# Kernel optimization log

Measured on AMD Instinct MI355X. Metric: run time of the kernel, lower is better.

## Reference

```python
import jax, jax.numpy as jnp
import numpy as np

N_NODES = 100000


def gcn_conv(x, W, b, src, dst, n):
    # PyG GCNConv: linear transform, add self-loops, symmetric deg^-1/2 norm,
    # scatter-sum messages from src -> dst, add bias.
    x = x @ W  # [N, out]
    loop = jnp.arange(n, dtype=src.dtype)
    src_sl = jnp.concatenate([src, loop])
    dst_sl = jnp.concatenate([dst, loop])
    deg = jax.ops.segment_sum(jnp.ones_like(dst_sl, dtype=x.dtype), dst_sl, num_segments=n)
    dinv = jax.lax.rsqrt(deg)
    norm = dinv[src_sl] * dinv[dst_sl]  # [E+N]
    msg = x[src_sl] * norm[:, None]
    out = jax.ops.segment_sum(msg, dst_sl, num_segments=n)
    return out + b


def base_gnn(x, edge_index, W1, b1, W2, b2):
    src, dst = edge_index[0], edge_index[1]
    n = x.shape[0]
    h = gcn_conv(x, W1, b1, src, dst, n)
    h = jax.nn.relu(h)
    return gcn_conv(h, W2, b2, src, dst, n)


def setup_inputs() -> dict:
    key = jax.random.key(0)
    ks = jax.random.split(key, 12)
    n, e, ep, en = N_NODES, 1600000, 200000, 200000
    in_ch, hid, out_ch, n_classes = 256, 128, 128, 10
    x = jax.random.normal(ks[0], (n, in_ch), dtype=jnp.float32)
    edge_index = jax.random.randint(ks[1], (2, e), 0, n, dtype=jnp.int64)
    edge_index_pos = jax.random.randint(ks[2], (2, ep), 0, n, dtype=jnp.int64)
    edge_index_neg = jax.random.randint(ks[3], (2, en), 0, n, dtype=jnp.int64)
    s1 = 1.0 / np.sqrt(in_ch)
    s2 = 1.0 / np.sqrt(hid)
    so = 1.0 / np.sqrt(out_ch)
    sl = 1.0 / np.sqrt(2 * out_ch)
    return {
        "x": x,
        "edge_index": edge_index,
        "edge_index_pos": edge_index_pos,
        "edge_index_neg": edge_index_neg,
        "W1": jax.random.uniform(ks[4], (in_ch, hid), jnp.float32, -s1, s1),
        "b1": jnp.zeros((hid,), jnp.float32),
        "W2": jax.random.uniform(ks[5], (hid, out_ch), jnp.float32, -s2, s2),
        "b2": jnp.zeros((out_ch,), jnp.float32),
        "Wcls": jax.random.uniform(ks[6], (out_ch, n_classes), jnp.float32, -so, so),
        "bcls": jax.random.uniform(ks[7], (n_classes,), jnp.float32, -so, so),
        "Wlink": jax.random.uniform(ks[8], (2 * out_ch, 1), jnp.float32, -sl, sl),
        "blink": jax.random.uniform(ks[9], (1,), jnp.float32, -sl, sl),
    }


def reference(x, edge_index, edge_index_pos, edge_index_neg,
              W1, b1, W2, b2, Wcls, bcls, Wlink, blink):
    # Shared base embedding (math identical to torch's redundant recompute)
    h = base_gnn(x, edge_index, W1, b1, W2, b2)  # [N, 128]
    # Node head
    node_logits = jax.nn.relu(h) @ Wcls + bcls
    node_pred = jax.nn.log_softmax(node_logits, axis=1)
    # Link head: gather endpoint embeddings, concat, linear
    xp = jnp.concatenate([h[edge_index_pos[0]], h[edge_index_pos[1]]], axis=1)
    xn = jnp.concatenate([h[edge_index_neg[0]], h[edge_index_neg[1]]], axis=1)
    link_pos = (xp @ Wlink + blink)[:, 0]
    link_neg = (xn @ Wlink + blink)[:, 0]
    return (node_pred, link_pos, link_neg)
```

## Files before the change

kernel.cpp:

```cpp
#include <hip/hip_runtime.h>
#include <stdint.h>

typedef __attribute__((ext_vector_type(8))) short bf16x8;
typedef __attribute__((ext_vector_type(4))) float f32x4;

__device__ __forceinline__ float b2f(uint32_t h) {
    union { uint32_t u; float f; } v; v.u = h << 16; return v.f;
}
__device__ __forceinline__ ushort f2b(float f) {
    union { float f; uint32_t u; } v; v.f = f;
    uint32_t u = v.u;
    return (ushort)((u + 0x7fffu + ((u >> 16) & 1u)) >> 16);
}
__device__ __forceinline__ float ldin(const void* p, int i, int fp32) {
    return fp32 ? ((const float*)p)[i] : b2f(((const ushort*)p)[i]);
}

__device__ __forceinline__ void sniff(const void* W1, const void* ei, int* sf) {
    if (threadIdx.x < 64) {
        int l = threadIdx.x;
        const ushort* w = (const ushort*)W1;
        bool bad = !(fabsf(b2f(w[l])) <= 0.25f) || !(fabsf(b2f(w[64 + l])) <= 0.25f);
        unsigned long long mb = __ballot(bad);
        const int* e = (const int*)ei;
        bool z = (l < 16) ? (e[2 * l + 1] == 0) : false;
        unsigned long long mz = __ballot(z);
        if (l == 0) {
            sf[0] = mb ? 1 : 0;
            sf[1] = (__popcll(mz & 0xffffull) >= 15) ? 1 : 0;
        }
    }
    __syncthreads();
}


__global__ __launch_bounds__(256) void k_prep(const void* ei, const void* ep, const void* en,
                                              const void* W1, const void* b1, const void* W2,
                                              const void* b2, const void* Wc, const void* bc,
                                              const void* Wl, const void* bl,
                                              int* cEi, int* cEp, int* cEn,
                                              ushort* Wt1, ushort* Wt2, ushort* WtC,
                                              ushort* b1c, ushort* b2c, ushort* bcc,
                                              ushort* Wlc, ushort* blc,
                                              int* __restrict__ histM,
                                              int twoEp, int twoEn, int N,
                                              int E, int NB1,
                                              int Bidx, int Bw) {
    __shared__ int sf[2];
    __shared__ int h[512];
    sniff(W1, ei, sf);
    int f = sf[0], i64 = sf[1];
    int b = blockIdx.x;

    if (b < Bidx) {
        int i = (b * 256 + threadIdx.x) * 2;
        const void* srcp; int* dstp; int j = i;
        if (i < E) { srcp = ei; dstp = cEi; }
        else if (i < E + twoEp) { srcp = ep; dstp = cEp; j = i - E; }
        else if (i < E + twoEp + twoEn) { srcp = en; dstp = cEn; j = i - E - twoEp; }
        else return;
        int v0, v1;
        if (i64) {
            longlong2 t = *(const longlong2*)((const long long*)srcp + j);
            v0 = (int)t.x; v1 = (int)t.y;
        } else {
            int2 t = *(const int2*)((const int*)srcp + j);
            v0 = t.x; v1 = t.y;
        }
        v0 = v0 < 0 ? 0 : (v0 >= N ? N - 1 : v0);
        v1 = v1 < 0 ? 0 : (v1 >= N ? N - 1 : v1);
        *(int2*)(dstp + j) = make_int2(v0, v1);
    } else if (b < Bidx + Bw) {
        int i = (b - Bidx) * 256 + threadIdx.x;
        if (i < 32768) {
            int c = i >> 8, kpos = i & 255;
            int s = kpos >> 5, t = kpos & 31, q = t >> 3, jj = t & 7;
            int k = s * 32 + (jj < 4 ? q * 4 + jj : 16 + q * 4 + (jj - 4));
            Wt1[i] = f2b(ldin(W1, k * 128 + c, f));
        } else if (i < 49152) {
            int j = i - 32768, c = j >> 7, k = j & 127;
            Wt2[j] = f2b(ldin(W2, k * 128 + c, f));
        } else if (i < 51200) {
            int j = i - 49152, c = j >> 7, k = j & 127;
            ushort v = 0;
            if (c < 10) v = f2b(ldin(Wc, k * 10 + c, f));
            WtC[j] = v;
        } else if (i < 51328) {
            int j = i - 51200; b1c[j] = f2b(ldin(b1, j, f));
        } else if (i < 51456) {
            int j = i - 51328; b2c[j] = f2b(ldin(b2, j, f));
        } else if (i < 51472) {
            int j = i - 51456;
            ushort v = 0;
            if (j < 10) v = f2b(ldin(bc, j, f));
            bcc[j] = v;
        } else if (i < 51728) {
            int j = i - 51472; Wlc[j] = f2b(ldin(Wl, j, f));
        } else if (i < 51736) {
            int j = i - 51728;
            ushort v = 0;
            if (j < 1) v = f2b(ldin(bl, 0, f));
            blc[j] = v;
        }
    } else {
        int b2 = b - Bidx - Bw;
        for (int j = threadIdx.x; j < 512; j += 256) h[j] = 0;
        __syncthreads();
        int base = b2 * 4096;
        for (int j = threadIdx.x; j < 4096; j += 256) {
            int i = base + j;
            if (i < E) {
                int d = i64 ? (int)((const long long*)ei)[E + i] : ((const int*)ei)[E + i];
                d = d < 0 ? 0 : (d >= N ? N - 1 : d);
                cEi[E + i] = d;
                atomicAdd(&h[d >> 8], 1);
            }
        }
        __syncthreads();
        for (int j = threadIdx.x; j < 512; j += 256)
            histM[j * NB1 + b2] = h[j];
    }
}

__global__ __launch_bounds__(1024) void k_mscan_block(const int* __restrict__ in, int* __restrict__ out,
                                                      int* __restrict__ bsum, int len) {
    __shared__ int sh[1024];
    int t = threadIdx.x;
    int i = blockIdx.x * 1024 + t;
    int val = (i < len) ? in[i] : 0;
    sh[t] = val; __syncthreads();
    for (int off = 1; off < 1024; off <<= 1) {
        int v = (t >= off) ? sh[t - off] : 0;
        __syncthreads();
        sh[t] += v;
        __syncthreads();
    }
    if (i < len) out[i] = sh[t] - val;
    if (t == 1023) bsum[blockIdx.x] = sh[1023];
}

__global__ __launch_bounds__(1024) void k_mscan_topadd(int* __restrict__ out, const int* __restrict__ bsum,
                                                       int* __restrict__ cbs, int len, int mb,
                                                       int NB1, int E) {
    __shared__ int sh[1024];
    int t = threadIdx.x;
    sh[t] = (t < mb) ? bsum[t] : 0; __syncthreads();
    for (int off = 1; off < 1024; off <<= 1) {
        int v = (t >= off) ? sh[t - off] : 0;
        __syncthreads();
        sh[t] += v;
        __syncthreads();
    }
    int pref = (blockIdx.x > 0) ? sh[blockIdx.x - 1] : 0;
    int i = blockIdx.x * 1024 + t;
    if (i < len) {
        int v = out[i] + pref;
        out[i] = v;
        if (i % NB1 == 0) cbs[i / NB1] = v;
    }
    if (i == 0) cbs[512] = E;
}

__global__ __launch_bounds__(256) void k_scatter1(const int* __restrict__ src, const int* __restrict__ dst,
                                                  const int* __restrict__ off, int2* __restrict__ grouped,
                                                  int E, int NB1) {
    __shared__ int o[512];
    for (int j = threadIdx.x; j < 512; j += 256) o[j] = off[j * NB1 + blockIdx.x];
    __syncthreads();
    int base = blockIdx.x * 4096;
    for (int j = threadIdx.x; j < 4096; j += 256) {
        int i = base + j;
        if (i < E) {
            int d = dst[i];
            int p = atomicAdd(&o[d >> 8], 1);
            grouped[p] = make_int2(src[i], d);
        }
    }
}

__global__ __launch_bounds__(256) void k_degfill(const int2* __restrict__ grouped, const int* __restrict__ cbs,
                                                 int* __restrict__ rowptr, float* __restrict__ dinv,
                                                 int* __restrict__ edgeS, int N, int E) {
    __shared__ int cnt[256];
    __shared__ int obase[256];
    int t = threadIdx.x, b = blockIdx.x;
    cnt[t] = 0;
    __syncthreads();
    int s0 = cbs[b], s1 = cbs[b + 1];
    for (int i = s0 + t; i < s1; i += 256)
        atomicAdd(&cnt[grouped[i].y & 255], 1);
    __syncthreads();
    int deg = cnt[t];
    __syncthreads();
    for (int off = 1; off < 256; off <<= 1) {
        int vv = (t >= off) ? cnt[t - off] : 0;
        __syncthreads();
        cnt[t] += vv;
        __syncthreads();
    }
    int excl = cnt[t] - deg;
    int v = b * 256 + t;
    if (v < N) {
        rowptr[v] = s0 + excl;
        dinv[v] = rsqrtf((float)(deg + 1));
    }
    if (b == 0 && t == 0) rowptr[N] = E;
    obase[t] = s0 + excl;
    __syncthreads();
    for (int i = s0 + t; i < s1; i += 256) {
        int2 e = grouped[i];
        int p = atomicAdd(&obase[e.y & 255], 1);
        edgeS[p] = e.x;
    }
}

template <int NS, bool FUSE>
__global__ __launch_bounds__(256) void k_gemm(const void* __restrict__ Xraw,
                                              const ushort* __restrict__ Wt,
                                              ushort* __restrict__ Out, int nrows,
                                              const void* W1s, const void* eis) {
    __shared__ int sf[2];
    sniff(W1s, eis, sf);
    const bool f32in = FUSE && sf[0];

    __shared__ uint4 sB[NS * 8 * 64];
    const int tid = threadIdx.x;
    for (int it = tid; it < NS * 8 * 64; it += 256) {
        int l = it & 63, fn = it >> 6;
        int s = fn >> 3, n = fn & 7;
        int mr = l & 15, q = l >> 4;
        sB[it] = *(const uint4*)(Wt + (size_t)(n * 16 + mr) * (NS * 32) + s * 32 + q * 8);
    }
    __syncthreads();

    const int wave = tid >> 6;
    const int l = tid & 63;
    const int q = l >> 4, mr = l & 15;
    const int gw = blockIdx.x * 4 + wave;
    const int nw = gridDim.x * 4;
    const int ntile = (nrows + 15) >> 4;
    const int K = NS * 32;

    for (int tp = gw; tp * 4 < ntile; tp += nw) {
        const int t0 = tp * 4;
        const bool h1 = (t0 + 1 < ntile), h2 = (t0 + 2 < ntile), h3 = (t0 + 3 < ntile);
        const int tb1 = h1 ? t0 + 1 : t0, tb2 = h2 ? t0 + 2 : t0, tb3 = h3 ? t0 + 3 : t0;

        int r0 = t0 * 16 + mr;  if (r0 > nrows - 1) r0 = nrows - 1;
        int r1 = tb1 * 16 + mr; if (r1 > nrows - 1) r1 = nrows - 1;
        int r2 = tb2 * 16 + mr; if (r2 > nrows - 1) r2 = nrows - 1;
        int r3 = tb3 * 16 + mr; if (r3 > nrows - 1) r3 = nrows - 1;

        f32x4 accA[8], accB[8], accC[8], accD[8];
#pragma unroll
        for (int n = 0; n < 8; ++n) {
            accA[n] = (f32x4){0.f, 0.f, 0.f, 0.f};
            accB[n] = (f32x4){0.f, 0.f, 0.f, 0.f};
            accC[n] = (f32x4){0.f, 0.f, 0.f, 0.f};
            accD[n] = (f32x4){0.f, 0.f, 0.f, 0.f};
        }
#pragma unroll
        for (int s = 0; s < NS; ++s) {
            bf16x8 a0, a1, a2, a3;
            if (FUSE) {
                if (f32in) {
                    const float* x0 = (const float*)Xraw + (size_t)r0 * K + s * 32;
                    const float* x1 = (const float*)Xraw + (size_t)r1 * K + s * 32;
                    const float* x2 = (const float*)Xraw + (size_t)r2 * K + s * 32;
                    const float* x3 = (const float*)Xraw + (size_t)r3 * K + s * 32;
                    float4 lo, hi;
#define LOADCVT(dst, xp)                                                        \
                    lo = *(const float4*)((xp) + q * 4);                        \
                    hi = *(const float4*)((xp) + 16 + q * 4);                   \
                    dst[0] = (short)f2b(lo.x); dst[1] = (short)f2b(lo.y);       \
                    dst[2] = (short)f2b(lo.z); dst[3] = (short)f2b(lo.w);       \
                    dst[4] = (short)f2b(hi.x); dst[5] = (short)f2b(hi.y);       \
                    dst[6] = (short)f2b(hi.z); dst[7] = (short)f2b(hi.w);
                    LOADCVT(a0, x0) LOADCVT(a1, x1) LOADCVT(a2, x2) LOADCVT(a3, x3)
#undef LOADCVT
                } else {
                    const ushort* x0 = (const ushort*)Xraw + (size_t)r0 * K + s * 32;
                    const ushort* x1 = (const ushort*)Xraw + (size_t)r1 * K + s * 32;
                    const ushort* x2 = (const ushort*)Xraw + (size_t)r2 * K + s * 32;
                    const ushort* x3 = (const ushort*)Xraw + (size_t)r3 * K + s * 32;
                    uint2 lo, hi; uint4 m;
#define LOADB(dst, xp)                                                          \
                    lo = *(const uint2*)((xp) + q * 4);                         \
                    hi = *(const uint2*)((xp) + 16 + q * 4);                    \
                    m = (uint4){lo.x, lo.y, hi.x, hi.y};                        \
                    dst = __builtin_bit_cast(bf16x8, m);
                    LOADB(a0, x0) LOADB(a1, x1) LOADB(a2, x2) LOADB(a3, x3)
#undef LOADB
                }
            } else {
                const ushort* Xf = (const ushort*)Xraw;
                a0 = *(const bf16x8*)(Xf + ((size_t)t0 * NS * 64 + l) * 8 + s * 512);
                a1 = *(const bf16x8*)(Xf + ((size_t)tb1 * NS * 64 + l) * 8 + s * 512);
                a2 = *(const bf16x8*)(Xf + ((size_t)tb2 * NS * 64 + l) * 8 + s * 512);
                a3 = *(const bf16x8*)(Xf + ((size_t)tb3 * NS * 64 + l) * 8 + s * 512);
            }
#pragma unroll
            for (int n = 0; n < 8; ++n) {
                bf16x8 bfr = __builtin_bit_cast(bf16x8, sB[(s * 8 + n) * 64 + l]);
                accA[n] = __builtin_amdgcn_mfma_f32_16x16x32_bf16(bfr, a0, accA[n], 0, 0, 0);
                accB[n] = __builtin_amdgcn_mfma_f32_16x16x32_bf16(bfr, a1, accB[n], 0, 0, 0);
                accC[n] = __builtin_amdgcn_mfma_f32_16x16x32_bf16(bfr, a2, accC[n], 0, 0, 0);
                accD[n] = __builtin_amdgcn_mfma_f32_16x16x32_bf16(bfr, a3, accD[n], 0, 0, 0);
            }
        }
        {
            int row = t0 * 16 + mr;
            if (row < nrows) {
                ushort* orow = Out + (size_t)row * 128 + q * 4;
#pragma unroll
                for (int n = 0; n < 8; ++n) {
                    uint2 o;
                    o.x = (uint32_t)f2b(accA[n][0]) | ((uint32_t)f2b(accA[n][1]) << 16);
                    o.y = (uint32_t)f2b(accA[n][2]) | ((uint32_t)f2b(accA[n][3]) << 16);
                    *(uint2*)(orow + n * 16) = o;
                }
            }
        }
        if (h1) {
            int row = tb1 * 16 + mr;
            if (row < nrows) {
                ushort* orow = Out + (size_t)row * 128 + q * 4;
#pragma unroll
                for (int n = 0; n < 8; ++n) {
                    uint2 o;
                    o.x = (uint32_t)f2b(accB[n][0]) | ((uint32_t)f2b(accB[n][1]) << 16);
                    o.y = (uint32_t)f2b(accB[n][2]) | ((uint32_t)f2b(accB[n][3]) << 16);
                    *(uint2*)(orow + n * 16) = o;
                }
            }
        }
        if (h2) {
            int row = tb2 * 16 + mr;
            if (row < nrows) {
                ushort* orow = Out + (size_t)row * 128 + q * 4;
#pragma unroll
                for (int n = 0; n < 8; ++n) {
                    uint2 o;
                    o.x = (uint32_t)f2b(accC[n][0]) | ((uint32_t)f2b(accC[n][1]) << 16);
                    o.y = (uint32_t)f2b(accC[n][2]) | ((uint32_t)f2b(accC[n][3]) << 16);
                    *(uint2*)(orow + n * 16) = o;
                }
            }
        }
        if (h3) {
            int row = tb3 * 16 + mr;
            if (row < nrows) {
                ushort* orow = Out + (size_t)row * 128 + q * 4;
#pragma unroll
                for (int n = 0; n < 8; ++n) {
                    uint2 o;
                    o.x = (uint32_t)f2b(accD[n][0]) | ((uint32_t)f2b(accD[n][1]) << 16);
                    o.y = (uint32_t)f2b(accD[n][2]) | ((uint32_t)f2b(accD[n][3]) << 16);
                    *(uint2*)(orow + n * 16) = o;
                }
            }
        }
    }
}

__device__ __forceinline__ void fma8(float* acc, uint4 p, float w) {
    uint32_t pu[4] = {p.x, p.y, p.z, p.w};
#pragma unroll
    for (int k = 0; k < 4; ++k) {
        float lo = __uint_as_float(pu[k] << 16);
        float hi = __uint_as_float(pu[k] & 0xffff0000u);
        acc[2 * k]     += lo * w;
        acc[2 * k + 1] += hi * w;
    }
}

__global__ __launch_bounds__(256) void k_conv(const ushort* __restrict__ XW, const int* __restrict__ rowptr,
                                              const int* __restrict__ edgeS, const float* __restrict__ dinv,
                                              const ushort* __restrict__ bias, ushort* __restrict__ Hout,
                                              int n, int relu, int frag) {
    int wave = threadIdx.x >> 6;
    int v = blockIdx.x * 4 + wave;
    if (v >= n) return;
    int l = threadIdx.x & 63;
    int g = l >> 4;
    int c = l & 15;

    int s0 = rowptr[v], s1 = rowptr[v + 1];
    float dv = dinv[v];
    float wself = (g == 0) ? dv * dv : 0.f;

    uint4 pv = *(const uint4*)(XW + (size_t)v * 128 + c * 8);
    float acc[8];
    {
        uint32_t pu[4] = {pv.x, pv.y, pv.z, pv.w};
#pragma unroll
        for (int k = 0; k < 4; ++k) {
            acc[2 * k]     = __uint_as_float(pu[k] << 16) * wself;
            acc[2 * k + 1] = __uint_as_float(pu[k] & 0xffff0000u) * wself;
        }
    }

    int i = s0;
    while (i + 16 <= s1) {
        int sA = edgeS[i + g];
        int sB = edgeS[i + 4 + g];
        int sC = edgeS[i + 8 + g];
        int sD = edgeS[i + 12 + g];
        uint4 pA = *(const uint4*)(XW + (size_t)sA * 128 + c * 8);
        uint4 pB = *(const uint4*)(XW + (size_t)sB * 128 + c * 8);
        uint4 pC = *(const uint4*)(XW + (size_t)sC * 128 + c * 8);
        uint4 pD = *(const uint4*)(XW + (size_t)sD * 128 + c * 8);
        float wA = dinv[sA] * dv, wB = dinv[sB] * dv;
        float wC = dinv[sC] * dv, wD = dinv[sD] * dv;
        fma8(acc, pA, wA);
        fma8(acc, pB, wB);
        fma8(acc, pC, wC);
        fma8(acc, pD, wD);
        i += 16;
    }
    if (i + 8 <= s1) {
        int sA = edgeS[i + g];
        int sB = edgeS[i + 4 + g];
        uint4 pA = *(const uint4*)(XW + (size_t)sA * 128 + c * 8);
        uint4 pB = *(const uint4*)(XW + (size_t)sB * 128 + c * 8);
        float wA = dinv[sA] * dv, wB = dinv[sB] * dv;
        fma8(acc, pA, wA);
        fma8(acc, pB, wB);
        i += 8;
    }
    if (i + 4 <= s1) {
        int sA = edgeS[i + g];
        uint4 pA = *(const uint4*)(XW + (size_t)sA * 128 + c * 8);
        fma8(acc, pA, dinv[sA] * dv);
        i += 4;
    }
    if (i < s1) {
        int ei_ = i + g;
        bool val = ei_ < s1;
        int sA = edgeS[val ? ei_ : s0];
        uint4 pA = *(const uint4*)(XW + (size_t)sA * 128 + c * 8);
        fma8(acc, pA, val ? dinv[sA] * dv : 0.f);
    }

#pragma unroll
    for (int k = 0; k < 8; ++k) {
        acc[k] += __shfl_xor(acc[k], 16);
        acc[k] += __shfl_xor(acc[k], 32);
    }

    if (g == 0) {
        uint4 bb = *(const uint4*)(bias + c * 8);
        uint32_t bu[4] = {bb.x, bb.y, bb.z, bb.w};
        uint4 o;
        uint32_t* op = (uint32_t*)&o;
#pragma unroll
        for (int k = 0; k < 4; ++k) {
            float lo = acc[2 * k]     + __uint_as_float(bu[k] << 16);
            float hi = acc[2 * k + 1] + __uint_as_float(bu[k] & 0xffff0000u);
            if (relu) { lo = fmaxf(lo, 0.f); hi = fmaxf(hi, 0.f); }
            op[k] = (uint32_t)f2b(lo) | ((uint32_t)f2b(hi) << 16);
        }
        if (frag) {
            int tile = v >> 4, mr = v & 15;
            size_t chunk = ((size_t)(tile * 4 + (c >> 2)) * 64 + (c & 3) * 16 + mr);
            *(uint4*)(Hout + chunk * 8) = o;
        } else {
            *(uint4*)(Hout + (size_t)v * 128 + c * 8) = o;
        }
    }
}

__global__ __launch_bounds__(256) void k_nodehead(const ushort* __restrict__ H, const ushort* __restrict__ WtC,
                                                  const ushort* __restrict__ bcc, const ushort* __restrict__ Wlc,
                                                  float2* __restrict__ ab, void* __restrict__ out,
                                                  int n, const void* W1s, const void* eis) {
    __shared__ int sf[2];
    sniff(W1s, eis, sf);
    int fp32o = sf[0];
    int wave = threadIdx.x >> 6;
    int gw = blockIdx.x * 4 + wave;
    if (gw * 16 >= n) return;
    int l = threadIdx.x & 63;
    int q = l >> 4, mr = l & 15;
    int m0 = gw * 16;

    const ushort* hrow = H + (size_t)(m0 + mr) * 128 + q * 8;
    bf16x8 araw[4];
#pragma unroll
    for (int s = 0; s < 4; ++s) araw[s] = *(const bf16x8*)(hrow + s * 32);

    float pa = 0.f, pb = 0.f;
#pragma unroll
    for (int s = 0; s < 4; ++s) {
        bf16x8 w0 = *(const bf16x8*)(Wlc + s * 32 + q * 8);
        bf16x8 w1 = *(const bf16x8*)(Wlc + 128 + s * 32 + q * 8);
#pragma unroll
        for (int j = 0; j < 8; ++j) {
            float hv = b2f((ushort)araw[s][j]);
            pa += hv * b2f((ushort)w0[j]);
            pb += hv * b2f((ushort)w1[j]);
        }
    }
    pa += __shfl_xor(pa, 16); pa += __shfl_xor(pa, 32);
    pb += __shfl_xor(pb, 16); pb += __shfl_xor(pb, 32);
    if (q == 0 && (m0 + mr) < n) ab[m0 + mr] = make_float2(pa, pb);

    f32x4 acc = (f32x4){0.f, 0.f, 0.f, 0.f};
#pragma unroll
    for (int s = 0; s < 4; ++s) {
        bf16x8 a = araw[s];
#pragma unroll
        for (int j = 0; j < 8; ++j) {
            ushort t = (ushort)a[j];
            if (t & 0x8000u) a[j] = 0;
        }
        bf16x8 b = *(const bf16x8*)(WtC + (size_t)mr * 128 + s * 32 + q * 8);
        acc = __builtin_amdgcn_mfma_f32_16x16x32_bf16(a, b, acc, 0, 0, 0);
    }

    float bc = b2f(bcc[mr]);
#pragma unroll
    for (int r = 0; r < 4; ++r) {
        float logit = acc[r] + bc;
        float m = (mr < 10) ? logit : -1e30f;
#pragma unroll
        for (int off = 1; off < 16; off <<= 1) m = fmaxf(m, __shfl_xor(m, off, 16));
        float ex = (mr < 10) ? expf(logit - m) : 0.f;
        float ssum = ex;
#pragma unroll
        for (int off = 1; off < 16; off <<= 1) ssum += __shfl_xor(ssum, off, 16);
        int row = m0 + q * 4 + r;
        if (mr < 10 && row < n) {
            float lsm = logit - m - logf(ssum);
            size_t idx = (size_t)row * 10 + mr;
            if (fp32o) ((float*)out)[idx] = lsm;
            else ((ushort*)out)[idx] = f2b(lsm);
        }
    }
}

__global__ __launch_bounds__(256) void k_linkfast(const float2* __restrict__ ab, const int* __restrict__ pos,
                                                  const int* __restrict__ neg, const ushort* __restrict__ blc,
                                                  void* __restrict__ out, size_t obase, int Ep, int En,
                                                  const void* W1s, const void* eis) {
    __shared__ int sf[2];
    sniff(W1s, eis, sf);
    int i = blockIdx.x * 256 + threadIdx.x;
    if (i >= Ep + En) return;
    int s, d;
    if (i < Ep) { s = pos[i]; d = pos[Ep + i]; }
    else { int j = i - Ep; s = neg[j]; d = neg[En + j]; }
    float vf = ab[s].x + ab[d].y + b2f(blc[0]);
    size_t idx = obase + (size_t)i;
    if (sf[0]) ((float*)out)[idx] = vf;
    else ((ushort*)out)[idx] = f2b(vf);
}

extern "C" void kernel_launch(void* const* d_in, const int* in_sizes, int n_in,
                              void* d_out, int out_size, void* d_ws, size_t ws_size,
                              hipStream_t stream) {
    const void* x    = d_in[0];
    const void* ei   = d_in[1];
    const void* eip  = d_in[2];
    const void* ein  = d_in[3];
    const void* W1   = d_in[4];
    const void* b1   = d_in[5];
    const void* W2   = d_in[6];
    const void* b2   = d_in[7];
    const void* Wcls = d_in[8];
    const void* bcls = d_in[9];
    const void* Wl   = d_in[10];
    const void* bl   = d_in[11];

    const int N  = in_sizes[0] / 256;
    const int E  = in_sizes[1] / 2;
    const int Ep = in_sizes[2] / 2;
    const int En = in_sizes[3] / 2;

    const int NB1  = (E + 4095) / 4096;
    const int mlen = 512 * NB1;
    const int mb   = (mlen + 1023) / 1024;
    const int ntile = (N + 15) / 16;

    char* ws = (char*)d_ws;
    size_t off = 0;
    auto alloc = [&](size_t bytes) -> void* {
        void* p = ws + off;
        off = (off + bytes + 255) & ~(size_t)255;
        return p;
    };
    ushort* bufXW  = (ushort*)alloc((size_t)N * 128 * 2);
    ushort* bufH   = (ushort*)alloc((size_t)ntile * 4 * 64 * 16);
    float2* ab     = (float2*)alloc((size_t)N * 8);
    int*    cEi    = (int*)alloc((size_t)2 * E * 4);
    int*    cEp    = (int*)alloc((size_t)2 * Ep * 4);
    int*    cEn    = (int*)alloc((size_t)2 * En * 4);
    int2*   grouped= (int2*)alloc((size_t)E * 8);
    int*    histM  = (int*)alloc((size_t)mlen * 4);
    int*    offM   = (int*)alloc((size_t)mlen * 4);
    int*    msum   = (int*)alloc(4096);
    int*    cbs    = (int*)alloc(513 * 4);
    float*  dinv   = (float*)alloc((size_t)N * 4);
    int*    rowp   = (int*)alloc((size_t)(N + 1) * 4);
    int*    edgeS  = (int*)alloc((size_t)E * 4);
    ushort* Wt1    = (ushort*)alloc(65536);
    ushort* Wt2    = (ushort*)alloc(32768);
    ushort* WtC    = (ushort*)alloc(4096);
    ushort* b1c    = (ushort*)alloc(256);
    ushort* b2c    = (ushort*)alloc(256);
    ushort* bcc    = (ushort*)alloc(64);
    ushort* Wlc    = (ushort*)alloc(512);
    ushort* blc    = (ushort*)alloc(64);

    int twoEp = 2 * Ep, twoEn = 2 * En;
    int idx_total = E + twoEp + twoEn;
    int Bidx = (idx_total + 511) / 512;
    int Bw   = 203;

    k_prep<<<Bidx + Bw + NB1, 256, 0, stream>>>(ei, eip, ein, W1, b1, W2, b2, Wcls, bcls, Wl, bl,
                                                cEi, cEp, cEn, Wt1, Wt2, WtC,
                                                b1c, b2c, bcc, Wlc, blc, histM,
                                                twoEp, twoEn, N, E, NB1,
                                                Bidx, Bw);

    const int* srcp = cEi;
    const int* dstp = cEi + E;

    k_mscan_block<<<mb, 1024, 0, stream>>>(histM, offM, msum, mlen);
    k_mscan_topadd<<<mb, 1024, 0, stream>>>(offM, msum, cbs, mlen, mb, NB1, E);
    k_scatter1<<<NB1, 256, 0, stream>>>(srcp, dstp, offM, grouped, E, NB1);
    k_degfill<<<512, 256, 0, stream>>>(grouped, cbs, rowp, dinv, edgeS, N, E);

    int quads = (ntile + 3) / 4;
    int g1 = (quads + 3) / 4; if (g1 > 768) g1 = 768;
    k_gemm<8, true><<<g1, 256, 0, stream>>>(x, Wt1, bufXW, N, W1, ei);
    k_conv<<<(N + 3) / 4, 256, 0, stream>>>(bufXW, rowp, edgeS, dinv, b1c, bufH, N, 1, 1);
    k_gemm<4, false><<<g1, 256, 0, stream>>>(bufH, Wt2, bufXW, N, W1, ei);
    k_conv<<<(N + 3) / 4, 256, 0, stream>>>(bufXW, rowp, edgeS, dinv, b2c, bufH, N, 0, 0);

    int head_blocks = ((N + 15) / 16 + 3) / 4;
    k_nodehead<<<head_blocks, 256, 0, stream>>>(bufH, WtC, bcc, Wlc, ab, d_out, N, W1, ei);
    k_linkfast<<<(Ep + En + 255) / 256, 256, 0, stream>>>(ab, cEp, cEn, blc, d_out,
                                                          (size_t)N * 10, Ep, En, W1, ei);
}
```

Baseline: 447.4 us.

## Drop shared-memory weight staging and shrink GEMM tile to two row-tiles per wave

The GEMM kernel no longer copies the weight matrix into LDS at block start. Weight fragments are now read straight from global memory (expected to hit in L1/L2) inside the MFMA loop. Each wave now handles 2 row tiles instead of 4, which halves accumulator registers and may raise occupancy. The grid is no longer capped at 768 blocks, so it grows to cover all tile pairs. The trade-off is less reuse of each weight load and more global and cache traffic for the weights, in exchange for removing the LDS prologue and barrier and lowering register pressure.

```diff
diff --git a/kernel.cpp b/kernel.cpp
--- a/kernel.cpp
+++ b/kernel.cpp
@@ -223,16 +223,7 @@
     sniff(W1s, eis, sf);
     const bool f32in = FUSE && sf[0];
 
-    __shared__ uint4 sB[NS * 8 * 64];
     const int tid = threadIdx.x;
-    for (int it = tid; it < NS * 8 * 64; it += 256) {
-        int l = it & 63, fn = it >> 6;
-        int s = fn >> 3, n = fn & 7;
-        int mr = l & 15, q = l >> 4;
-        sB[it] = *(const uint4*)(Wt + (size_t)(n * 16 + mr) * (NS * 32) + s * 32 + q * 8);
-    }
-    __syncthreads();
-
     const int wave = tid >> 6;
     const int l = tid & 63;
     const int q = l >> 4, mr = l & 15;
@@ -241,33 +232,27 @@
     const int ntile = (nrows + 15) >> 4;
     const int K = NS * 32;
 
-    for (int tp = gw; tp * 4 < ntile; tp += nw) {
-        const int t0 = tp * 4;
-        const bool h1 = (t0 + 1 < ntile), h2 = (t0 + 2 < ntile), h3 = (t0 + 3 < ntile);
-        const int tb1 = h1 ? t0 + 1 : t0, tb2 = h2 ? t0 + 2 : t0, tb3 = h3 ? t0 + 3 : t0;
+    for (int tp = gw; tp * 2 < ntile; tp += nw) {
+        const int t0 = tp * 2;
+        const bool h1 = (t0 + 1 < ntile);
+        const int tb1 = h1 ? t0 + 1 : t0;
 
         int r0 = t0 * 16 + mr;  if (r0 > nrows - 1) r0 = nrows - 1;
         int r1 = tb1 * 16 + mr; if (r1 > nrows - 1) r1 = nrows - 1;
-        int r2 = tb2 * 16 + mr; if (r2 > nrows - 1) r2 = nrows - 1;
-        int r3 = tb3 * 16 + mr; if (r3 > nrows - 1) r3 = nrows - 1;
-
-        f32x4 accA[8], accB[8], accC[8], accD[8];
+
+        f32x4 accA[8], accB[8];
 #pragma unroll
         for (int n = 0; n < 8; ++n) {
             accA[n] = (f32x4){0.f, 0.f, 0.f, 0.f};
             accB[n] = (f32x4){0.f, 0.f, 0.f, 0.f};
-            accC[n] = (f32x4){0.f, 0.f, 0.f, 0.f};
-            accD[n] = (f32x4){0.f, 0.f, 0.f, 0.f};
         }
 #pragma unroll
         for (int s = 0; s < NS; ++s) {
-            bf16x8 a0, a1, a2, a3;
+            bf16x8 a0, a1;
             if (FUSE) {
                 if (f32in) {
                     const float* x0 = (const float*)Xraw + (size_t)r0 * K + s * 32;
                     const float* x1 = (const float*)Xraw + (size_t)r1 * K + s * 32;
-                    const float* x2 = (const float*)Xraw + (size_t)r2 * K + s * 32;
-                    const float* x3 = (const float*)Xraw + (size_t)r3 * K + s * 32;
                     float4 lo, hi;
 #define LOADCVT(dst, xp)                                                        \
                     lo = *(const float4*)((xp) + q * 4);                        \
@@ -276,36 +261,30 @@
                     dst[2] = (short)f2b(lo.z); dst[3] = (short)f2b(lo.w);       \
                     dst[4] = (short)f2b(hi.x); dst[5] = (short)f2b(hi.y);       \
                     dst[6] = (short)f2b(hi.z); dst[7] = (short)f2b(hi.w);
-                    LOADCVT(a0, x0) LOADCVT(a1, x1) LOADCVT(a2, x2) LOADCVT(a3, x3)
+                    LOADCVT(a0, x0) LOADCVT(a1, x1)
 #undef LOADCVT
                 } else {
                     const ushort* x0 = (const ushort*)Xraw + (size_t)r0 * K + s * 32;
                     const ushort* x1 = (const ushort*)Xraw + (size_t)r1 * K + s * 32;
-                    const ushort* x2 = (const ushort*)Xraw + (size_t)r2 * K + s * 32;
-                    const ushort* x3 = (const ushort*)Xraw + (size_t)r3 * K + s * 32;
                     uint2 lo, hi; uint4 m;
 #define LOADB(dst, xp)                                                          \
                     lo = *(const uint2*)((xp) + q * 4);                         \
                     hi = *(const uint2*)((xp) + 16 + q * 4);                    \
                     m = (uint4){lo.x, lo.y, hi.x, hi.y};                        \
                     dst = __builtin_bit_cast(bf16x8, m);
-                    LOADB(a0, x0) LOADB(a1, x1) LOADB(a2, x2) LOADB(a3, x3)
+                    LOADB(a0, x0) LOADB(a1, x1)
 #undef LOADB
                 }
             } else {
                 const ushort* Xf = (const ushort*)Xraw;
                 a0 = *(const bf16x8*)(Xf + ((size_t)t0 * NS * 64 + l) * 8 + s * 512);
                 a1 = *(const bf16x8*)(Xf + ((size_t)tb1 * NS * 64 + l) * 8 + s * 512);
-                a2 = *(const bf16x8*)(Xf + ((size_t)tb2 * NS * 64 + l) * 8 + s * 512);
-                a3 = *(const bf16x8*)(Xf + ((size_t)tb3 * NS * 64 + l) * 8 + s * 512);
             }
 #pragma unroll
             for (int n = 0; n < 8; ++n) {
-                bf16x8 bfr = __builtin_bit_cast(bf16x8, sB[(s * 8 + n) * 64 + l]);
+                bf16x8 bfr = *(const bf16x8*)(Wt + (size_t)(n * 16 + mr) * K + s * 32 + q * 8);
                 accA[n] = __builtin_amdgcn_mfma_f32_16x16x32_bf16(bfr, a0, accA[n], 0, 0, 0);
                 accB[n] = __builtin_amdgcn_mfma_f32_16x16x32_bf16(bfr, a1, accB[n], 0, 0, 0);
-                accC[n] = __builtin_amdgcn_mfma_f32_16x16x32_bf16(bfr, a2, accC[n], 0, 0, 0);
-                accD[n] = __builtin_amdgcn_mfma_f32_16x16x32_bf16(bfr, a3, accD[n], 0, 0, 0);
             }
         }
         {
@@ -330,32 +309,6 @@
                     uint2 o;
                     o.x = (uint32_t)f2b(accB[n][0]) | ((uint32_t)f2b(accB[n][1]) << 16);
                     o.y = (uint32_t)f2b(accB[n][2]) | ((uint32_t)f2b(accB[n][3]) << 16);
-                    *(uint2*)(orow + n * 16) = o;
-                }
-            }
-        }
-        if (h2) {
-            int row = tb2 * 16 + mr;
-            if (row < nrows) {
-                ushort* orow = Out + (size_t)row * 128 + q * 4;
-#pragma unroll
-                for (int n = 0; n < 8; ++n) {
-                    uint2 o;
-                    o.x = (uint32_t)f2b(accC[n][0]) | ((uint32_t)f2b(accC[n][1]) << 16);
-                    o.y = (uint32_t)f2b(accC[n][2]) | ((uint32_t)f2b(accC[n][3]) << 16);
-                    *(uint2*)(orow + n * 16) = o;
-                }
-            }
-        }
-        if (h3) {
-            int row = tb3 * 16 + mr;
-            if (row < nrows) {
-                ushort* orow = Out + (size_t)row * 128 + q * 4;
-#pragma unroll
-                for (int n = 0; n < 8; ++n) {
-                    uint2 o;
-                    o.x = (uint32_t)f2b(accD[n][0]) | ((uint32_t)f2b(accD[n][1]) << 16);
-                    o.y = (uint32_t)f2b(accD[n][2]) | ((uint32_t)f2b(accD[n][3]) << 16);
                     *(uint2*)(orow + n * 16) = o;
                 }
             }
@@ -631,11 +584,11 @@
     k_scatter1<<<NB1, 256, 0, stream>>>(srcp, dstp, offM, grouped, E, NB1);
     k_degfill<<<512, 256, 0, stream>>>(grouped, cbs, rowp, dinv, edgeS, N, E);
 
-    int quads = (ntile + 3) / 4;
-    int g1 = (quads + 3) / 4; if (g1 > 768) g1 = 768;
-    k_gemm<8, true><<<g1, 256, 0, stream>>>(x, Wt1, bufXW, N, W1, ei);
+    int pairs = (ntile + 1) / 2;
+    int gg = (pairs + 3) / 4;
+    k_gemm<8, true><<<gg, 256, 0, stream>>>(x, Wt1, bufXW, N, W1, ei);
     k_conv<<<(N + 3) / 4, 256, 0, stream>>>(bufXW, rowp, edgeS, dinv, b1c, bufH, N, 1, 1);
-    k_gemm<4, false><<<g1, 256, 0, stream>>>(bufH, Wt2, bufXW, N, W1, ei);
+    k_gemm<4, false><<<gg, 256, 0, stream>>>(bufH, Wt2, bufXW, N, W1, ei);
     k_conv<<<(N + 3) / 4, 256, 0, stream>>>(bufXW, rowp, edgeS, dinv, b2c, bufH, N, 0, 0);
 
     int head_blocks = ((N + 15) / 16 + 3) / 4;
```

Result: slower. 475.7 us (+6.3%).
